# Kernel tuning notes

Hardware: AMD Instinct MI355X
Metric: run time of the kernel (lower is better)

Reference implementation:

```python
import jax, jax.numpy as jnp
import numpy as np

B, L, D = 64, 512, 1024
C, O = 32, 64  # num_capsules, output_dim
ROUTING_ITERS = 3


def setup_inputs() -> dict:
    key = jax.random.key(0)
    k1, k2, k3 = jax.random.split(key, 3)
    inputs = jax.random.normal(k1, (B, L, D), dtype=jnp.float32)
    # nn.Linear(input_dim, num_capsules*output_dim): weight stored as (out, in) in torch;
    # we store the transposed (in, out) form for a clean matmul.
    bound = 1.0 / np.sqrt(D)
    fc_w = jax.random.uniform(k2, (D, C * O), dtype=jnp.float32, minval=-bound, maxval=bound)
    fc_b = jax.random.uniform(k3, (C * O,), dtype=jnp.float32, minval=-bound, maxval=bound)
    return {"inputs": inputs, "fc_w": fc_w, "fc_b": fc_b}


def squash(x):
    # x: (..., O)
    sq = jnp.sum(x * x, axis=-1, keepdims=True)
    scale = sq / (1.0 + sq)
    return scale * x / jnp.sqrt(sq + 1e-8)


def reference(inputs, fc_w, fc_b):
    b, l = inputs.shape[0], inputs.shape[1]
    # Transformer: linear projection to capsule predictions u_hat (B, L, C, O)
    u_hat = (jnp.einsum('bld,dk->blk', inputs, fc_w) + fc_b).reshape(b, l, C, O)
    b_ij = jnp.zeros((b, l, C), dtype=inputs.dtype)
    v_j = None
    for _ in range(ROUTING_ITERS):
        c_ij = jax.nn.softmax(b_ij, axis=2)                 # (B, L, C)
        s_j = jnp.einsum('blc,blco->bco', c_ij, u_hat)      # (B, C, O)
        v_j = squash(s_j)                                    # (B, C, O)
        b_ij = b_ij + jnp.einsum('blco,bco->blc', u_hat, v_j)
    return v_j
```

## Files before the change

### kernel.cpp

```cpp
#include <hip/hip_runtime.h>


namespace {
constexpr int Bn = 64, Ln = 512, Dn = 1024, Cn = 32, On = 64, COn = Cn * On;
}

typedef float f32x4 __attribute__((ext_vector_type(4)));
typedef short bf16x8 __attribute__((ext_vector_type(8)));

static __device__ __forceinline__ unsigned f2bf(float f) {
    unsigned u = __float_as_uint(f);
    u += 0x7fff + ((u >> 16) & 1);
    return u >> 16;
}

__global__ __launch_bounds__(256) void k_ctr(const float* __restrict__ in,
                                             short* __restrict__ in_bf,
                                             float* __restrict__ rs_p) {
    int b = blockIdx.y;
    int lc = blockIdx.x >> 2, ds = blockIdx.x & 3;
    int l0 = lc * 64, d0 = ds * 256;
    int t = threadIdx.x, w = t >> 6, lane = t & 63;
    int db = lane & 7, lb = lane >> 3;
    int dloc = w * 64 + db * 8;
    int lloc = lb * 8;

    const float* src = in + ((size_t)b * Ln + l0 + lloc) * Dn + d0 + dloc;
    float4 ld[8][2];
#pragma unroll
    for (int r = 0; r < 8; ++r) {
        ld[r][0] = *(const float4*)(src + (size_t)r * Dn);
        ld[r][1] = *(const float4*)(src + (size_t)r * Dn + 4);
    }
    unsigned mr[8][4];
    float s[8];
#pragma unroll
    for (int k = 0; k < 8; ++k) s[k] = 0.f;
#pragma unroll
    for (int r = 0; r < 8; ++r) {
        const float* e = (const float*)&ld[r][0];
#pragma unroll
        for (int j = 0; j < 4; ++j)
            mr[r][j] = f2bf(e[2 * j]) | (f2bf(e[2 * j + 1]) << 16);
#pragma unroll
        for (int k = 0; k < 8; ++k) s[k] += e[k];
    }
    short* dbf = in_bf + ((size_t)b * Ln + l0 + lloc) * Dn + d0 + dloc;
#pragma unroll
    for (int r = 0; r < 8; ++r)
        *(uint4*)(dbf + (size_t)r * Dn) = make_uint4(mr[r][0], mr[r][1], mr[r][2], mr[r][3]);
#pragma unroll
    for (int k = 0; k < 8; ++k) {
        s[k] += __shfl_xor(s[k], 8, 64);
        s[k] += __shfl_xor(s[k], 16, 64);
        s[k] += __shfl_xor(s[k], 32, 64);
    }
    if (lb == 0) {
        float* rp = rs_p + ((size_t)b * 8 + lc) * Dn + d0 + dloc;
        *(float4*)rp = make_float4(s[0], s[1], s[2], s[3]);
        *(float4*)(rp + 4) = make_float4(s[4], s[5], s[6], s[7]);
    }
}

__global__ __launch_bounds__(256) void k_prep2(const float* __restrict__ fc_w,
                                               short* __restrict__ fc_wT,
                                               short* __restrict__ fc_wb,
                                               const float* __restrict__ rs_p,
                                               unsigned short* __restrict__ rs_bf) {
    __shared__ short tr[64 * 260];
    int t = threadIdx.x;
    if (blockIdx.x < 128) {
        int id = blockIdx.x;
        int d0 = (id & 15) * 64;
        int co0 = (id >> 4) * 256;
        int grp = t >> 6, cq = t & 63;
#pragma unroll
        for (int i = 0; i < 16; ++i) {
            int row = grp + 4 * i;
            float4 x = *(const float4*)(fc_w + (size_t)(d0 + row) * COn + co0 + cq * 4);
            short4 s4 = make_short4((short)f2bf(x.x), (short)f2bf(x.y),
                                    (short)f2bf(x.z), (short)f2bf(x.w));
            *(short4*)(&tr[row * 260 + cq * 4]) = s4;
            *(short4*)(fc_wb + (size_t)(d0 + row) * COn + co0 + cq * 4) = s4;
        }
        __syncthreads();
#pragma unroll
        for (int i = 0; i < 8; ++i) {
            int idx = t + 256 * i;
            int corow = idx >> 3, slot = idx & 7;
            bf16x8 v;
#pragma unroll
            for (int j = 0; j < 8; ++j) v[j] = tr[(slot * 8 + j) * 260 + corow];
            *(bf16x8*)(fc_wT + (size_t)(co0 + corow) * Dn + d0 + slot * 8) = v;
        }
    } else {
        int id = blockIdx.x - 128;
        int b = id >> 2, dq = id & 3;
        int d = dq * 256 + t;
        float s = 0.f;
#pragma unroll
        for (int lc = 0; lc < 8; ++lc) s += rs_p[((size_t)b * 8 + lc) * Dn + d];
        rs_bf[b * Dn + d] = (unsigned short)f2bf(s * (1.0f / 32.0f));
    }
}

__global__ __launch_bounds__(64) void k_sv3(const short* __restrict__ xA,
                                            const float* __restrict__ csum_p,
                                            const short* __restrict__ fc_wT,
                                            const float* __restrict__ fc_b,
                                            short* __restrict__ v_bf,
                                            float* __restrict__ fout,
                                            float* __restrict__ bias_v,
                                            int mode0) {
    int w = blockIdx.x;
    int c = blockIdx.y;
    int lane = threadIdx.x;
    int l15 = lane & 15, lg = lane >> 4;
    const short* A = mode0 ? xA : (xA + (size_t)c * Bn * Dn);
    const short* Bw = fc_wT + (size_t)c * On * Dn;
    f32x4 acc[4];
#pragma unroll
    for (int i = 0; i < 4; ++i) acc[i] = {0.f, 0.f, 0.f, 0.f};
#pragma unroll 4
    for (int ks = 0; ks < 32; ++ks) {
        int koff = ks * 32 + lg * 8;
        bf16x8 a = *(const bf16x8*)(A + (size_t)(w * 16 + l15) * Dn + koff);
#pragma unroll
        for (int dt = 0; dt < 4; ++dt) {
            bf16x8 bbf = *(const bf16x8*)(Bw + (size_t)(dt * 16 + l15) * Dn + koff);
            acc[dt] = __builtin_amdgcn_mfma_f32_16x16x32_bf16(a, bbf, acc[dt], 0, 0, 0);
        }
    }
    float fb[4];
#pragma unroll
    for (int dt = 0; dt < 4; ++dt) fb[dt] = fc_b[c * On + dt * 16 + l15];
#pragma unroll
    for (int r = 0; r < 4; ++r) {
        int brow = w * 16 + lg * 4 + r;
        float cs;
        if (mode0) {
            cs = 16.0f;
        } else {
            cs = 0.f;
#pragma unroll
            for (int lt = 0; lt < 8; ++lt) cs += csum_p[((size_t)lt * Bn + brow) * Cn + c];
        }
        float s0 = acc[0][r] + cs * fb[0];
        float s1 = acc[1][r] + cs * fb[1];
        float s2 = acc[2][r] + cs * fb[2];
        float s3 = acc[3][r] + cs * fb[3];
        float sq = s0 * s0 + s1 * s1 + s2 * s2 + s3 * s3;
        sq += __shfl_xor(sq, 1, 64); sq += __shfl_xor(sq, 2, 64);
        sq += __shfl_xor(sq, 4, 64); sq += __shfl_xor(sq, 8, 64);
        float scale = sq / (1.0f + sq) * rsqrtf(sq + 1e-8f);
        float v0 = scale * s0, v1 = scale * s1, v2 = scale * s2, v3 = scale * s3;
        size_t vo = ((size_t)brow * Cn + c) * On;
        v_bf[vo + 0 * 16 + l15] = (short)f2bf(v0);
        v_bf[vo + 1 * 16 + l15] = (short)f2bf(v1);
        v_bf[vo + 2 * 16 + l15] = (short)f2bf(v2);
        v_bf[vo + 3 * 16 + l15] = (short)f2bf(v3);
        if (fout) {
            fout[vo + 0 * 16 + l15] = v0;
            fout[vo + 1 * 16 + l15] = v1;
            fout[vo + 2 * 16 + l15] = v2;
            fout[vo + 3 * 16 + l15] = v3;
        }
        float bv = fb[0] * v0 + fb[1] * v1 + fb[2] * v2 + fb[3] * v3;
        bv += __shfl_xor(bv, 1, 64); bv += __shfl_xor(bv, 2, 64);
        bv += __shfl_xor(bv, 4, 64); bv += __shfl_xor(bv, 8, 64);
        if (l15 == 0) bias_v[brow * Cn + c] = bv;
    }
}

__global__ __launch_bounds__(256) void k_wv_m(const short* __restrict__ fc_wb,
                                              const short* __restrict__ v_bf,
                                              short* __restrict__ w_vb) {
    int dsl = blockIdx.x, c = blockIdx.y;
    int t = threadIdx.x, w = t >> 6, lane = t & 63;
    int l15 = lane & 15, lg = lane >> 4;
    int dbase = dsl * 256 + w * 64;
    f32x4 acc[4][4];
#pragma unroll
    for (int i = 0; i < 4; ++i)
#pragma unroll
        for (int j = 0; j < 4; ++j) acc[i][j] = {0.f, 0.f, 0.f, 0.f};
#pragma unroll
    for (int ks = 0; ks < 2; ++ks) {
        int o = ks * 32 + lg * 8;
        bf16x8 bfr[4];
#pragma unroll
        for (int nt = 0; nt < 4; ++nt)
            bfr[nt] = *(const bf16x8*)(v_bf + ((size_t)(nt * 16 + l15) * Cn + c) * On + o);
#pragma unroll
        for (int mt = 0; mt < 4; ++mt) {
            bf16x8 a = *(const bf16x8*)(fc_wb + (size_t)(dbase + mt * 16 + l15) * COn + c * On + o);
#pragma unroll
            for (int nt = 0; nt < 4; ++nt)
                acc[mt][nt] = __builtin_amdgcn_mfma_f32_16x16x32_bf16(a, bfr[nt], acc[mt][nt], 0, 0, 0);
        }
    }
#pragma unroll
    for (int mt = 0; mt < 4; ++mt)
#pragma unroll
        for (int nt = 0; nt < 4; ++nt) {
            int bb = nt * 16 + l15;
            int d = dbase + mt * 16 + lg * 4;
            *(short4*)(w_vb + ((size_t)bb * Cn + c) * Dn + d) =
                make_short4((short)f2bf(acc[mt][nt][0]), (short)f2bf(acc[mt][nt][1]),
                            (short)f2bf(acc[mt][nt][2]), (short)f2bf(acc[mt][nt][3]));
        }
}

__global__ __launch_bounds__(256) void k_route_m(const short* __restrict__ in_bf,
                                                 const short* __restrict__ w_v,
                                                 const float* __restrict__ bias_v,
                                                 float* __restrict__ b_ij,
                                                 short* __restrict__ c_wT,
                                                 float* __restrict__ csum_p,
                                                 int first, int last) {
    __shared__ short cw_sh[Cn * 68];
    __shared__ float cs_sh[4][Cn];
    int lt = blockIdx.x, b = blockIdx.y;
    int t = threadIdx.x, w = t >> 6, lane = t & 63;
    int l15 = lane & 15, lg = lane >> 4;
    int l0 = lt * 64;
    f32x4 acc0 = {0.f, 0.f, 0.f, 0.f}, acc1 = {0.f, 0.f, 0.f, 0.f};
    const short* Ap = in_bf + ((size_t)b * Ln + l0 + w * 16 + l15) * Dn;
    const short* Bp = w_v + (size_t)b * Cn * Dn;
#pragma unroll 4
    for (int ks = 0; ks < 32; ++ks) {
        int koff = ks * 32 + lg * 8;
        bf16x8 a = *(const bf16x8*)(Ap + koff);
        bf16x8 b0 = *(const bf16x8*)(Bp + (size_t)l15 * Dn + koff);
        bf16x8 b1 = *(const bf16x8*)(Bp + (size_t)(l15 + 16) * Dn + koff);
        acc0 = __builtin_amdgcn_mfma_f32_16x16x32_bf16(a, b0, acc0, 0, 0, 0);
        acc1 = __builtin_amdgcn_mfma_f32_16x16x32_bf16(a, b1, acc1, 0, 0, 0);
    }
    float bv0 = bias_v[b * Cn + l15];
    float bv1 = bias_v[b * Cn + l15 + 16];
    float csa0 = 0.f, csa1 = 0.f;
#pragma unroll
    for (int r = 0; r < 4; ++r) {
        int lrow = l0 + w * 16 + lg * 4 + r;
        size_t boff = ((size_t)b * Ln + lrow) * Cn;
        float d0 = acc0[r] + bv0, d1 = acc1[r] + bv1;
        if (!first) { d0 += b_ij[boff + l15]; d1 += b_ij[boff + l15 + 16]; }
        if (!last) {
            b_ij[boff + l15] = d0;
            b_ij[boff + l15 + 16] = d1;
        }
        float m = fmaxf(d0, d1);
        m = fmaxf(m, __shfl_xor(m, 1, 64)); m = fmaxf(m, __shfl_xor(m, 2, 64));
        m = fmaxf(m, __shfl_xor(m, 4, 64)); m = fmaxf(m, __shfl_xor(m, 8, 64));
        float e0 = __expf(d0 - m), e1 = __expf(d1 - m);
        float sm = e0 + e1;
        sm += __shfl_xor(sm, 1, 64); sm += __shfl_xor(sm, 2, 64);
        sm += __shfl_xor(sm, 4, 64); sm += __shfl_xor(sm, 8, 64);
        float inv = 1.0f / sm;
        float cw0 = e0 * inv, cw1 = e1 * inv;
        csa0 += cw0; csa1 += cw1;
        int ll = w * 16 + lg * 4 + r;
        cw_sh[l15 * 68 + ll] = (short)f2bf(cw0);
        cw_sh[(l15 + 16) * 68 + ll] = (short)f2bf(cw1);
    }
    csa0 += __shfl_xor(csa0, 16, 64); csa0 += __shfl_xor(csa0, 32, 64);
    csa1 += __shfl_xor(csa1, 16, 64); csa1 += __shfl_xor(csa1, 32, 64);
    if (lg == 0) { cs_sh[w][l15] = csa0; cs_sh[w][l15 + 16] = csa1; }
    __syncthreads();
    if (t < Cn) {
        float s = cs_sh[0][t] + cs_sh[1][t] + cs_sh[2][t] + cs_sh[3][t];
        csum_p[((size_t)lt * Bn + b) * Cn + t] = s;
    }
    {
        int cc = t >> 3, slot = t & 7;
        bf16x8 vv;
#pragma unroll
        for (int j = 0; j < 8; ++j) vv[j] = cw_sh[cc * 68 + slot * 8 + j];
        *(bf16x8*)(c_wT + ((size_t)b * Cn + cc) * Ln + l0 + slot * 8) = vv;
    }
}

__global__ __launch_bounds__(256) void k_xc_m(const short* __restrict__ in_bf,
                                              const short* __restrict__ c_wT,
                                              short* __restrict__ x_cb) {
    __shared__ unsigned tile[128 * 36];
    int dt = blockIdx.x, b = blockIdx.y;
    int t = threadIdx.x, w = t >> 6, lane = t & 63;
    int l15 = lane & 15, lg = lane >> 4;
    f32x4 acc[2][2];
#pragma unroll
    for (int h = 0; h < 2; ++h)
#pragma unroll
        for (int dd = 0; dd < 2; ++dd) acc[h][dd] = {0.f, 0.f, 0.f, 0.f};
    const short* A = c_wT + (size_t)b * Cn * Ln;

    int oct = t & 15, lpA = t >> 4, lpB = lpA + 16;
    const short* gbase = in_bf + (size_t)b * Ln * Dn + dt * 128 + oct * 8;
    int colA = lpA ^ ((oct & 7) << 2);
    int colB = lpB ^ ((oct & 7) << 2);
    unsigned* trow = &tile[(oct * 8) * 36];

    bf16x8 ra0, ra1, rb0, rb1;
    bf16x8 a0c[2], a1c[2], a0n[2], a1n[2];

#define XC_LOADG(LC)                                                          \
    {                                                                         \
        const short* sA = gbase + (size_t)((LC) * 64 + 2 * lpA) * Dn;         \
        const short* sB = gbase + (size_t)((LC) * 64 + 2 * lpB) * Dn;         \
        ra0 = *(const bf16x8*)sA; ra1 = *(const bf16x8*)(sA + Dn);            \
        rb0 = *(const bf16x8*)sB; rb1 = *(const bf16x8*)(sB + Dn);            \
    }
#define XC_LOADA(LC, D0, D1)                                                  \
    _Pragma("unroll")                                                         \
    for (int ks = 0; ks < 2; ++ks) {                                          \
        int off = (LC) * 64 + ks * 32 + lg * 8;                               \
        D0[ks] = *(const bf16x8*)(A + (size_t)l15 * Ln + off);                \
        D1[ks] = *(const bf16x8*)(A + (size_t)(l15 + 16) * Ln + off);         \
    }

    XC_LOADG(0);
    XC_LOADA(0, a0c, a1c);

    for (int lc = 0; lc < 8; ++lc) {
#pragma unroll
        for (int k = 0; k < 8; ++k) {
            trow[k * 36 + colA] = (unsigned)(unsigned short)ra0[k] |
                                  ((unsigned)(unsigned short)ra1[k] << 16);
            trow[k * 36 + colB] = (unsigned)(unsigned short)rb0[k] |
                                  ((unsigned)(unsigned short)rb1[k] << 16);
        }
        __syncthreads();
        if (lc < 7) {
            XC_LOADG(lc + 1);
            XC_LOADA(lc + 1, a0n, a1n);
        }
#pragma unroll
        for (int ks = 0; ks < 2; ++ks) {
            int q = ks * 4 + lg;
#pragma unroll
            for (int dd = 0; dd < 2; ++dd) {
                int dloc = w * 32 + dd * 16 + l15;
                int qs = q ^ ((dloc >> 3) & 7);
                bf16x8 bb = *(const bf16x8*)&tile[dloc * 36 + qs * 4];
                acc[0][dd] = __builtin_amdgcn_mfma_f32_16x16x32_bf16(a0c[ks], bb, acc[0][dd], 0, 0, 0);
                acc[1][dd] = __builtin_amdgcn_mfma_f32_16x16x32_bf16(a1c[ks], bb, acc[1][dd], 0, 0, 0);
            }
        }
        __syncthreads();
        if (lc < 7) {
#pragma unroll
            for (int ks = 0; ks < 2; ++ks) { a0c[ks] = a0n[ks]; a1c[ks] = a1n[ks]; }
        }
    }
#undef XC_LOADG
#undef XC_LOADA
#pragma unroll
    for (int h = 0; h < 2; ++h)
#pragma unroll
        for (int dd = 0; dd < 2; ++dd)
#pragma unroll
            for (int r = 0; r < 4; ++r) {
                int c = 16 * h + lg * 4 + r;
                int d = dt * 128 + w * 32 + dd * 16 + l15;
                x_cb[((size_t)c * Bn + b) * Dn + d] = (short)f2bf(acc[h][dd][r]);
            }
}

extern "C" void kernel_launch(void* const* d_in, const int* in_sizes, int n_in,
                              void* d_out, int out_size, void* d_ws, size_t ws_size,
                              hipStream_t stream) {
    const float* in   = (const float*)d_in[0];
    const float* fc_w = (const float*)d_in[1];
    const float* fc_b = (const float*)d_in[2];
    float* out = (float*)d_out;

    char* p = (char*)d_ws;
    auto alloc = [&](size_t bytes) -> char* {
        char* r = p;
        p += (bytes + 255) & ~(size_t)255;
        return r;
    };
    short* in_bf  = (short*)alloc((size_t)Bn * Ln * Dn * 2);
    short* fc_wT  = (short*)alloc((size_t)COn * Dn * 2);
    short* fc_wb  = (short*)alloc((size_t)COn * Dn * 2);
    short* w_vb   = (short*)alloc((size_t)Bn * Cn * Dn * 2);
    short* c_wT   = (short*)alloc((size_t)Bn * Cn * Ln * 2);
    short* x_cb   = (short*)alloc((size_t)Cn * Bn * Dn * 2);
    short* v_bf   = (short*)alloc((size_t)Bn * Cn * On * 2);
    float* rs_p   = (float*)alloc((size_t)Bn * 8 * Dn * 4);
    unsigned short* rs_bf = (unsigned short*)alloc((size_t)Bn * Dn * 2);
    float* b_ij   = (float*)alloc((size_t)Bn * Ln * Cn * 4);
    float* bias_v = (float*)alloc((size_t)Bn * Cn * 4);
    float* csum_p = (float*)alloc((size_t)8 * Bn * Cn * 4);

    k_ctr<<<dim3(32, Bn), 256, 0, stream>>>(in, in_bf, rs_p);
    k_prep2<<<384, 256, 0, stream>>>(fc_w, fc_wT, fc_wb, rs_p, rs_bf);
    k_sv3<<<dim3(4, Cn), 64, 0, stream>>>((const short*)rs_bf, csum_p, fc_wT,
                                          fc_b, v_bf, nullptr, bias_v, 1);
    for (int it = 1; it <= 2; ++it) {
        k_wv_m<<<dim3(4, Cn), 256, 0, stream>>>(fc_wb, v_bf, w_vb);
        k_route_m<<<dim3(8, Bn), 256, 0, stream>>>(in_bf, w_vb, bias_v, b_ij,
                                                   c_wT, csum_p,
                                                   (it == 1) ? 1 : 0,
                                                   (it == 2) ? 1 : 0);
        k_xc_m<<<dim3(8, Bn), 256, 0, stream>>>(in_bf, c_wT, x_cb);
        k_sv3<<<dim3(4, Cn), 64, 0, stream>>>(x_cb, csum_p, fc_wT, fc_b,
                                              v_bf, (it == 2) ? out : nullptr,
                                              bias_v, 0);
    }
}
```

Before: 190.3 us.

## Split-K routing kernel over twice as many blocks; fold k_ctr d-slices into one block

```diff
diff --git a/kernel.cpp b/kernel.cpp
--- a/kernel.cpp
+++ b/kernel.cpp
@@ -17,48 +17,51 @@
 __global__ __launch_bounds__(256) void k_ctr(const float* __restrict__ in,
                                              short* __restrict__ in_bf,
                                              float* __restrict__ rs_p) {
-    int b = blockIdx.y;
-    int lc = blockIdx.x >> 2, ds = blockIdx.x & 3;
-    int l0 = lc * 64, d0 = ds * 256;
+    int lc = blockIdx.x, b = blockIdx.y;
+    int l0 = lc * 64;
     int t = threadIdx.x, w = t >> 6, lane = t & 63;
     int db = lane & 7, lb = lane >> 3;
-    int dloc = w * 64 + db * 8;
     int lloc = lb * 8;
-
-    const float* src = in + ((size_t)b * Ln + l0 + lloc) * Dn + d0 + dloc;
-    float4 ld[8][2];
-#pragma unroll
-    for (int r = 0; r < 8; ++r) {
-        ld[r][0] = *(const float4*)(src + (size_t)r * Dn);
-        ld[r][1] = *(const float4*)(src + (size_t)r * Dn + 4);
-    }
-    unsigned mr[8][4];
-    float s[8];
-#pragma unroll
-    for (int k = 0; k < 8; ++k) s[k] = 0.f;
-#pragma unroll
-    for (int r = 0; r < 8; ++r) {
-        const float* e = (const float*)&ld[r][0];
-#pragma unroll
-        for (int j = 0; j < 4; ++j)
-            mr[r][j] = f2bf(e[2 * j]) | (f2bf(e[2 * j + 1]) << 16);
-#pragma unroll
-        for (int k = 0; k < 8; ++k) s[k] += e[k];
-    }
-    short* dbf = in_bf + ((size_t)b * Ln + l0 + lloc) * Dn + d0 + dloc;
-#pragma unroll
-    for (int r = 0; r < 8; ++r)
-        *(uint4*)(dbf + (size_t)r * Dn) = make_uint4(mr[r][0], mr[r][1], mr[r][2], mr[r][3]);
-#pragma unroll
-    for (int k = 0; k < 8; ++k) {
-        s[k] += __shfl_xor(s[k], 8, 64);
-        s[k] += __shfl_xor(s[k], 16, 64);
-        s[k] += __shfl_xor(s[k], 32, 64);
-    }
-    if (lb == 0) {
-        float* rp = rs_p + ((size_t)b * 8 + lc) * Dn + d0 + dloc;
-        *(float4*)rp = make_float4(s[0], s[1], s[2], s[3]);
-        *(float4*)(rp + 4) = make_float4(s[4], s[5], s[6], s[7]);
+#pragma unroll
+    for (int ds = 0; ds < 4; ++ds) {
+        int d0 = ds * 256;
+        int dloc = w * 64 + db * 8;
+        const float* src = in + ((size_t)b * Ln + l0 + lloc) * Dn + d0 + dloc;
+        float4 ld[8][2];
+#pragma unroll
+        for (int r = 0; r < 8; ++r) {
+            ld[r][0] = *(const float4*)(src + (size_t)r * Dn);
+            ld[r][1] = *(const float4*)(src + (size_t)r * Dn + 4);
+        }
+        unsigned mr[8][4];
+        float s[8];
+#pragma unroll
+        for (int k = 0; k < 8; ++k) s[k] = 0.f;
+#pragma unroll
+        for (int r = 0; r < 8; ++r) {
+            const float* e = (const float*)&ld[r][0];
+#pragma unroll
+            for (int j = 0; j < 4; ++j)
+                mr[r][j] = f2bf(e[2 * j]) | (f2bf(e[2 * j + 1]) << 16);
+#pragma unroll
+            for (int k = 0; k < 8; ++k) s[k] += e[k];
+        }
+        short* dbf = in_bf + ((size_t)b * Ln + l0 + lloc) * Dn + d0 + dloc;
+#pragma unroll
+        for (int r = 0; r < 8; ++r)
+            *(uint4*)(dbf + (size_t)r * Dn) =
+                make_uint4(mr[r][0], mr[r][1], mr[r][2], mr[r][3]);
+#pragma unroll
+        for (int k = 0; k < 8; ++k) {
+            s[k] += __shfl_xor(s[k], 8, 64);
+            s[k] += __shfl_xor(s[k], 16, 64);
+            s[k] += __shfl_xor(s[k], 32, 64);
+        }
+        if (lb == 0) {
+            float* rp = rs_p + ((size_t)b * 8 + lc) * Dn + d0 + dloc;
+            *(float4*)rp = make_float4(s[0], s[1], s[2], s[3]);
+            *(float4*)(rp + 4) = make_float4(s[4], s[5], s[6], s[7]);
+        }
     }
 }
 
@@ -143,7 +146,7 @@
         } else {
             cs = 0.f;
 #pragma unroll
-            for (int lt = 0; lt < 8; ++lt) cs += csum_p[((size_t)lt * Bn + brow) * Cn + c];
+            for (int lt = 0; lt < 16; ++lt) cs += csum_p[((size_t)lt * Bn + brow) * Cn + c];
         }
         float s0 = acc[0][r] + cs * fb[0];
         float s1 = acc[1][r] + cs * fb[1];
@@ -211,24 +214,26 @@
         }
 }
 
-__global__ __launch_bounds__(256) void k_route_m(const short* __restrict__ in_bf,
-                                                 const short* __restrict__ w_v,
-                                                 const float* __restrict__ bias_v,
-                                                 float* __restrict__ b_ij,
-                                                 short* __restrict__ c_wT,
-                                                 float* __restrict__ csum_p,
-                                                 int first, int last) {
-    __shared__ short cw_sh[Cn * 68];
-    __shared__ float cs_sh[4][Cn];
-    int lt = blockIdx.x, b = blockIdx.y;
+__global__ __launch_bounds__(256) void k_route2(const short* __restrict__ in_bf,
+                                                const short* __restrict__ w_v,
+                                                const float* __restrict__ bias_v,
+                                                float* __restrict__ b_ij,
+                                                short* __restrict__ c_wT,
+                                                float* __restrict__ csum_p,
+                                                int first, int last) {
+    __shared__ float red[2][8][64];
+    __shared__ short cw_sh[Cn * 40];
+    __shared__ float cs_sh[2][Cn];
+    int lt2 = blockIdx.x, b = blockIdx.y;
     int t = threadIdx.x, w = t >> 6, lane = t & 63;
+    int lgrp = w >> 1, kh = w & 1;
     int l15 = lane & 15, lg = lane >> 4;
-    int l0 = lt * 64;
+    int l0 = lt2 * 32 + lgrp * 16;
     f32x4 acc0 = {0.f, 0.f, 0.f, 0.f}, acc1 = {0.f, 0.f, 0.f, 0.f};
-    const short* Ap = in_bf + ((size_t)b * Ln + l0 + w * 16 + l15) * Dn;
-    const short* Bp = w_v + (size_t)b * Cn * Dn;
+    const short* Ap = in_bf + ((size_t)b * Ln + l0 + l15) * Dn + kh * 512;
+    const short* Bp = w_v + (size_t)b * Cn * Dn + kh * 512;
 #pragma unroll 4
-    for (int ks = 0; ks < 32; ++ks) {
+    for (int ks = 0; ks < 16; ++ks) {
         int koff = ks * 32 + lg * 8;
         bf16x8 a = *(const bf16x8*)(Ap + koff);
         bf16x8 b0 = *(const bf16x8*)(Bp + (size_t)l15 * Dn + koff);
@@ -236,47 +241,62 @@
         acc0 = __builtin_amdgcn_mfma_f32_16x16x32_bf16(a, b0, acc0, 0, 0, 0);
         acc1 = __builtin_amdgcn_mfma_f32_16x16x32_bf16(a, b1, acc1, 0, 0, 0);
     }
-    float bv0 = bias_v[b * Cn + l15];
-    float bv1 = bias_v[b * Cn + l15 + 16];
-    float csa0 = 0.f, csa1 = 0.f;
-#pragma unroll
-    for (int r = 0; r < 4; ++r) {
-        int lrow = l0 + w * 16 + lg * 4 + r;
-        size_t boff = ((size_t)b * Ln + lrow) * Cn;
-        float d0 = acc0[r] + bv0, d1 = acc1[r] + bv1;
-        if (!first) { d0 += b_ij[boff + l15]; d1 += b_ij[boff + l15 + 16]; }
-        if (!last) {
-            b_ij[boff + l15] = d0;
-            b_ij[boff + l15 + 16] = d1;
-        }
-        float m = fmaxf(d0, d1);
-        m = fmaxf(m, __shfl_xor(m, 1, 64)); m = fmaxf(m, __shfl_xor(m, 2, 64));
-        m = fmaxf(m, __shfl_xor(m, 4, 64)); m = fmaxf(m, __shfl_xor(m, 8, 64));
-        float e0 = __expf(d0 - m), e1 = __expf(d1 - m);
-        float sm = e0 + e1;
-        sm += __shfl_xor(sm, 1, 64); sm += __shfl_xor(sm, 2, 64);
-        sm += __shfl_xor(sm, 4, 64); sm += __shfl_xor(sm, 8, 64);
-        float inv = 1.0f / sm;
-        float cw0 = e0 * inv, cw1 = e1 * inv;
-        csa0 += cw0; csa1 += cw1;
-        int ll = w * 16 + lg * 4 + r;
-        cw_sh[l15 * 68 + ll] = (short)f2bf(cw0);
-        cw_sh[(l15 + 16) * 68 + ll] = (short)f2bf(cw1);
-    }
-    csa0 += __shfl_xor(csa0, 16, 64); csa0 += __shfl_xor(csa0, 32, 64);
-    csa1 += __shfl_xor(csa1, 16, 64); csa1 += __shfl_xor(csa1, 32, 64);
-    if (lg == 0) { cs_sh[w][l15] = csa0; cs_sh[w][l15 + 16] = csa1; }
+    if (kh == 1) {
+#pragma unroll
+        for (int j = 0; j < 4; ++j) {
+            red[lgrp][j][lane] = acc0[j];
+            red[lgrp][4 + j][lane] = acc1[j];
+        }
+    }
+    __syncthreads();
+    if (kh == 0) {
+#pragma unroll
+        for (int j = 0; j < 4; ++j) {
+            acc0[j] += red[lgrp][j][lane];
+            acc1[j] += red[lgrp][4 + j][lane];
+        }
+        float bv0 = bias_v[b * Cn + l15];
+        float bv1 = bias_v[b * Cn + l15 + 16];
+        float csa0 = 0.f, csa1 = 0.f;
+#pragma unroll
+        for (int r = 0; r < 4; ++r) {
+            int lrow = l0 + lg * 4 + r;
+            size_t boff = ((size_t)b * Ln + lrow) * Cn;
+            float d0 = acc0[r] + bv0, d1 = acc1[r] + bv1;
+            if (!first) { d0 += b_ij[boff + l15]; d1 += b_ij[boff + l15 + 16]; }
+            if (!last) {
+                b_ij[boff + l15] = d0;
+                b_ij[boff + l15 + 16] = d1;
+            }
+            float m = fmaxf(d0, d1);
+            m = fmaxf(m, __shfl_xor(m, 1, 64)); m = fmaxf(m, __shfl_xor(m, 2, 64));
+            m = fmaxf(m, __shfl_xor(m, 4, 64)); m = fmaxf(m, __shfl_xor(m, 8, 64));
+            float e0 = __expf(d0 - m), e1 = __expf(d1 - m);
+            float sm = e0 + e1;
+            sm += __shfl_xor(sm, 1, 64); sm += __shfl_xor(sm, 2, 64);
+            sm += __shfl_xor(sm, 4, 64); sm += __shfl_xor(sm, 8, 64);
+            float inv = 1.0f / sm;
+            float cw0 = e0 * inv, cw1 = e1 * inv;
+            csa0 += cw0; csa1 += cw1;
+            int ll = lgrp * 16 + lg * 4 + r;
+            cw_sh[l15 * 40 + ll] = (short)f2bf(cw0);
+            cw_sh[(l15 + 16) * 40 + ll] = (short)f2bf(cw1);
+        }
+        csa0 += __shfl_xor(csa0, 16, 64); csa0 += __shfl_xor(csa0, 32, 64);
+        csa1 += __shfl_xor(csa1, 16, 64); csa1 += __shfl_xor(csa1, 32, 64);
+        if (lg == 0) { cs_sh[lgrp][l15] = csa0; cs_sh[lgrp][l15 + 16] = csa1; }
+    }
     __syncthreads();
     if (t < Cn) {
-        float s = cs_sh[0][t] + cs_sh[1][t] + cs_sh[2][t] + cs_sh[3][t];
-        csum_p[((size_t)lt * Bn + b) * Cn + t] = s;
-    }
-    {
-        int cc = t >> 3, slot = t & 7;
+        float s = cs_sh[0][t] + cs_sh[1][t];
+        csum_p[((size_t)lt2 * Bn + b) * Cn + t] = s;
+    }
+    if (t < 128) {
+        int cc = t >> 2, slot = t & 3;
         bf16x8 vv;
 #pragma unroll
-        for (int j = 0; j < 8; ++j) vv[j] = cw_sh[cc * 68 + slot * 8 + j];
-        *(bf16x8*)(c_wT + ((size_t)b * Cn + cc) * Ln + l0 + slot * 8) = vv;
+        for (int j = 0; j < 8; ++j) vv[j] = cw_sh[cc * 40 + slot * 8 + j];
+        *(bf16x8*)(c_wT + ((size_t)b * Cn + cc) * Ln + lt2 * 32 + slot * 8) = vv;
     }
 }
 
@@ -391,15 +411,15 @@
     unsigned short* rs_bf = (unsigned short*)alloc((size_t)Bn * Dn * 2);
     float* b_ij   = (float*)alloc((size_t)Bn * Ln * Cn * 4);
     float* bias_v = (float*)alloc((size_t)Bn * Cn * 4);
-    float* csum_p = (float*)alloc((size_t)8 * Bn * Cn * 4);
-
-    k_ctr<<<dim3(32, Bn), 256, 0, stream>>>(in, in_bf, rs_p);
+    float* csum_p = (float*)alloc((size_t)16 * Bn * Cn * 4);
+
+    k_ctr<<<dim3(8, Bn), 256, 0, stream>>>(in, in_bf, rs_p);
     k_prep2<<<384, 256, 0, stream>>>(fc_w, fc_wT, fc_wb, rs_p, rs_bf);
     k_sv3<<<dim3(4, Cn), 64, 0, stream>>>((const short*)rs_bf, csum_p, fc_wT,
                                           fc_b, v_bf, nullptr, bias_v, 1);
     for (int it = 1; it <= 2; ++it) {
         k_wv_m<<<dim3(4, Cn), 256, 0, stream>>>(fc_wb, v_bf, w_vb);
-        k_route_m<<<dim3(8, Bn), 256, 0, stream>>>(in_bf, w_vb, bias_v, b_ij,
+        k_route2<<<dim3(16, Bn), 256, 0, stream>>>(in_bf, w_vb, bias_v, b_ij,
                                                    c_wT, csum_p,
                                                    (it == 1) ? 1 : 0,
                                                    (it == 2) ? 1 : 0);
```

New measurement: 180.9 us. 5.0% less time.
